# Kernel optimization log

Hardware: AMD Instinct MI355X
Metric: run time of the kernel (lower is better)

The kernel has to match this reference:

```python
import jax, jax.numpy as jnp
import numpy as np

D_MODEL = 256
D_STATE = 64
R_MIN, R_MAX, MAX_PHASE = 0.0, 1.0, 6.28


def setup_inputs() -> dict:
    key = jax.random.key(0)
    ks = jax.random.split(key, 8)
    u1 = jax.random.uniform(ks[0], (D_STATE,), dtype=jnp.float32)
    u2 = jax.random.uniform(ks[1], (D_STATE,), dtype=jnp.float32)
    nu_log = jnp.log(-0.5 * jnp.log(u1 * (R_MAX**2 - R_MIN**2) + R_MIN**2))
    theta_log = jnp.log(u2 * MAX_PHASE)
    sB = 1.0 / np.sqrt(2 * D_STATE)
    sC = 1.0 / np.sqrt(D_STATE)
    B_re = jax.random.normal(ks[2], (D_MODEL, D_STATE), dtype=jnp.float32) * sB
    B_im = jax.random.normal(ks[3], (D_MODEL, D_STATE), dtype=jnp.float32) * sB
    C_re = jax.random.normal(ks[4], (D_MODEL, D_STATE), dtype=jnp.float32) * sC
    C_im = jax.random.normal(ks[5], (D_MODEL, D_STATE), dtype=jnp.float32) * sC
    D = jax.random.normal(ks[6], (D_MODEL,), dtype=jnp.float32)
    x = jax.random.normal(ks[7], (4, 8192, D_MODEL), dtype=jnp.float32)
    return {"x": x, "nu_log": nu_log, "theta_log": theta_log,
            "B_re": B_re, "B_im": B_im, "C_re": C_re, "C_im": C_im, "D": D}


def reference(x, nu_log, theta_log, B_re, B_im, C_re, C_im, D):
    B, L, H = x.shape
    # diagonal transition: Lambda = exp(-exp(nu) + i*exp(theta)); Lambda^k = exp(k*log_lambda)
    log_lambda = -jnp.exp(nu_log) + 1j * jnp.exp(theta_log)          # (n,)
    k = jnp.arange(L, dtype=jnp.float32)
    Lambda_k = jnp.exp(k[:, None] * log_lambda[None, :])              # (L, n) complex
    CB = (C_re + 1j * C_im) * (B_re + 1j * B_im)                      # (H, n)
    kernels = jnp.einsum('hn,ln->hl', CB, Lambda_k).real              # (H, L)
    # FFT (causal, linear) convolution per channel
    n_fft = 2 * L
    x_f = jnp.fft.rfft(x, n=n_fft, axis=1)                            # (B, L+1, H)
    k_f = jnp.fft.rfft(kernels, n=n_fft, axis=1)                      # (H, L+1)
    y_f = x_f * k_f.T[None]                                           # (B, L+1, H)
    y = jnp.fft.irfft(y_f, n=n_fft, axis=1)[:, :L, :]
    return y + x * D[None, None, :]
```

## Files before the change

### kernel.cpp

```cpp
#include <hip/hip_runtime.h>
#include <hip/hip_bf16.h>

#define BB   4
#define LL   8192
#define HH   256
#define NN   64
#define NSEG 128
#define LSEG 64

typedef __attribute__((ext_vector_type(8))) short  short8;
typedef __attribute__((ext_vector_type(4))) float  float4v;
typedef __attribute__((ext_vector_type(4))) int    int4v;


__device__ __forceinline__ float ldF(const void* p, size_t i, int isbf) {
    return isbf ? __bfloat162float(((const __hip_bfloat16*)p)[i])
                : ((const float*)p)[i];
}

__global__ void k_sniff(const void* p0, const void* p1, const void* p2,
                        const void* p3, const void* p4, const void* p5,
                        const void* p6, const void* p7, int* flags)
{
    int t = threadIdx.x;
    if (t < 8) {
        const void* ps[8] = {p0, p1, p2, p3, p4, p5, p6, p7};
        const unsigned int* d = (const unsigned int*)ps[t];
        int nbf = 0, nrand = 0;
        for (int i = 0; i < 32; ++i) {
            unsigned int lo = d[i] & 0xFFFFu;
            unsigned int e  = (lo >> 7) & 0xFFu;
            if (lo == 0u) {  }
            else if (e >= 90u && e <= 140u) nbf++;
            else nrand++;
        }
        flags[t] = (nrand == 0 && nbf >= 8) ? 1 : 0;
    }
}

__global__ __launch_bounds__(256) void k_setup(
    const void* nu_log, const void* theta_log,
    const void* B_re, const void* B_im,
    const void* C_re, const void* C_im,
    const void* D, const int* __restrict__ flags,
    float* lam, float* lam64, float* Df, float* CBt,
    float* PsegRe, float* PsegIm)
{
    int t = blockIdx.x * 256 + threadIdx.x;
    if (t < NN) {
        float nu = expf(ldF(nu_log, t, flags[1]));
        float th = expf(ldF(theta_log, t, flags[2]));
        float a  = expf(-nu);
        lam[2*t]   = a * cosf(th);
        lam[2*t+1] = a * sinf(th);
        float a64 = expf(-64.0f * nu);
        float ph  = 64.0f * th;
        lam64[2*t]   = a64 * cosf(ph);
        lam64[2*t+1] = a64 * sinf(ph);
    }
    if (t < HH) Df[t] = ldF(D, t, flags[7]);
    if (t < HH * NN) {
        int h = t >> 6, n = t & 63;
        float bre = ldF(B_re, h*NN+n, flags[3]);
        float bim = ldF(B_im, h*NN+n, flags[4]);
        float cre = ldF(C_re, h*NN+n, flags[5]);
        float cim = ldF(C_im, h*NN+n, flags[6]);
        CBt[(n*2+0)*HH + h] = cre*bre - cim*bim;
        CBt[(n*2+1)*HH + h] = cre*bim + cim*bre;
    }
    if (t < 64 * 64) {
        int l = t >> 6, n = t & 63;
        float nu = expf(ldF(nu_log, n, flags[1]));
        float th = expf(ldF(theta_log, n, flags[2]));
        float fp = (float)(63 - l);
        float ar = expf(-fp * nu);
        PsegRe[t] = ar * cosf(fp * th);
        PsegIm[t] = ar * sinf(fp * th);
    }
}

__global__ __launch_bounds__(256) void k_ktab(
    const float* __restrict__ CBt, const float* __restrict__ PsegRe,
    const float* __restrict__ PsegIm, const float* __restrict__ lam64,
    float* __restrict__ Ktab,
    short* __restrict__ VreT, short* __restrict__ VimnT,
    short* __restrict__ PreH, short* __restrict__ PreL,
    short* __restrict__ PimH, short* __restrict__ PimL)
{
    int t = blockIdx.x * 256 + threadIdx.x;
    int h = t >> 6, j = t & 63;
    float acc = 0.f;
    for (int n = 0; n < NN; ++n)
        acc += CBt[(2*n)*HH + h]   * PsegRe[(63-j)*64 + n]
             - CBt[(2*n+1)*HH + h] * PsegIm[(63-j)*64 + n];
    Ktab[j*HH + h] = acc;
    if (t < 64*64) {
        int tau = t >> 6, n = t & 63;
        float vr, vi;
        if (tau < 63) {
            vr =  PsegRe[(62-tau)*64 + n];
            vi = -PsegIm[(62-tau)*64 + n];
        } else {
            vr =  lam64[2*n];
            vi = -lam64[2*n+1];
        }
        __hip_bfloat16 br = __float2bfloat16(vr);
        __hip_bfloat16 bi = __float2bfloat16(vi);
        VreT[tau*64 + n]  = *(short*)&br;
        VimnT[tau*64 + n] = *(short*)&bi;

        int n2 = t >> 6, l2 = t & 63;
        float pr = PsegRe[l2*64 + n2];
        float pi = PsegIm[l2*64 + n2];
        __hip_bfloat16 prh = __float2bfloat16(pr);
        __hip_bfloat16 prl = __float2bfloat16(pr - __bfloat162float(prh));
        __hip_bfloat16 pih = __float2bfloat16(pi);
        __hip_bfloat16 pil = __float2bfloat16(pi - __bfloat162float(pih));
        PreH[t] = *(short*)&prh;
        PreL[t] = *(short*)&prl;
        PimH[t] = *(short*)&pih;
        PimL[t] = *(short*)&pil;
    }
}

template<bool ISBF>
__device__ __forceinline__ void segsum_body(
    const void* __restrict__ x, size_t xbase,
    const short* __restrict__ PreH, const short* __restrict__ PreL,
    const short* __restrict__ PimH, const short* __restrict__ PimL,
    __hip_bfloat16* __restrict__ Abuf, size_t abase, int q, int l15)
{
    #pragma unroll
    for (int nt = 0; nt < 4; ++nt) {
        short8 xh[2], xl[2];
        #pragma unroll
        for (int ks = 0; ks < 2; ++ks)
            #pragma unroll
            for (int j = 0; j < 8; ++j) {
                size_t a = xbase + nt*16 + (size_t)(ks*32 + q*8 + j)*HH;
                if (ISBF) {
                    xh[ks][j] = ((const short*)x)[a];
                } else {
                    float xf = ((const float*)x)[a];
                    __hip_bfloat16 hv = __float2bfloat16(xf);
                    __hip_bfloat16 lv = __float2bfloat16(xf - __bfloat162float(hv));
                    xh[ks][j] = *(short*)&hv;
                    xl[ks][j] = *(short*)&lv;
                }
            }
        #pragma unroll
        for (int mt = 0; mt < 4; ++mt) {
            float4v ar = {0.f, 0.f, 0.f, 0.f};
            float4v ai = {0.f, 0.f, 0.f, 0.f};
            #pragma unroll
            for (int ks = 0; ks < 2; ++ks) {
                int off = (mt*16 + l15)*64 + ks*32 + q*8;
                short8 prh = *(const short8*)(PreH + off);
                short8 pih = *(const short8*)(PimH + off);
                short8 prl = *(const short8*)(PreL + off);
                short8 pil = *(const short8*)(PimL + off);
                ar = __builtin_amdgcn_mfma_f32_16x16x32_bf16(prh, xh[ks], ar, 0, 0, 0);
                ai = __builtin_amdgcn_mfma_f32_16x16x32_bf16(pih, xh[ks], ai, 0, 0, 0);
                ar = __builtin_amdgcn_mfma_f32_16x16x32_bf16(prl, xh[ks], ar, 0, 0, 0);
                ai = __builtin_amdgcn_mfma_f32_16x16x32_bf16(pil, xh[ks], ai, 0, 0, 0);
                if (!ISBF) {
                    ar = __builtin_amdgcn_mfma_f32_16x16x32_bf16(prh, xl[ks], ar, 0, 0, 0);
                    ai = __builtin_amdgcn_mfma_f32_16x16x32_bf16(pih, xl[ks], ai, 0, 0, 0);
                }
            }
            #pragma unroll
            for (int r = 0; r < 4; ++r) {
                int n = mt*16 + q*4 + r;
                Abuf[abase + (size_t)n*128 + nt*16 + l15]      = __float2bfloat16(ar[r]);
                Abuf[abase + (size_t)n*128 + 64 + nt*16 + l15] = __float2bfloat16(ai[r]);
            }
        }
    }
}

__global__ __launch_bounds__(256) void k_segsum(
    const void* __restrict__ x,
    const short* __restrict__ PreH, const short* __restrict__ PreL,
    const short* __restrict__ PimH, const short* __restrict__ PimL,
    const int* __restrict__ flags, __hip_bfloat16* __restrict__ Abuf)
{
    int bk = blockIdx.x;
    int s  = bk & (NSEG - 1);
    int b  = bk >> 7;
    int w    = threadIdx.x >> 6;
    int lane = threadIdx.x & 63;
    int q = lane >> 4, l15 = lane & 15;

    size_t xbase = ((size_t)(b*LL) + s*64) * HH + w*64 + l15;
    size_t abase = (((size_t)(b*4 + w) * NSEG + s) * NN) * 128;

    if (flags[0]) segsum_body<true >(x, xbase, PreH, PreL, PimH, PimL, Abuf, abase, q, l15);
    else          segsum_body<false>(x, xbase, PreH, PreL, PimH, PimL, Abuf, abase, q, l15);
}

__global__ __launch_bounds__(256) void k_scan(
    const float* __restrict__ lam64, const float* __restrict__ CBt,
    __hip_bfloat16* __restrict__ Abuf)
{
    int w    = blockIdx.x * 4 + (threadIdx.x >> 6);
    int lane = threadIdx.x & 63;
    int n    = w & 63;
    int hg   = (w >> 6) & 3;
    int b    = w >> 8;
    int h    = hg*64 + lane;

    float lre = lam64[2*n], lim = lam64[2*n+1];
    float cbre = CBt[(2*n)*HH + h], cbim = CBt[(2*n+1)*HH + h];
    float sre = 0.f, sim = 0.f;
    size_t base0 = (((size_t)(b*4 + hg) * NSEG) * NN + n) * 128 + lane;

    float curR[16], curI[16], nxtR[16], nxtI[16];
    #pragma unroll
    for (int k = 0; k < 16; ++k) {
        size_t base = base0 + (size_t)k * NN * 128;
        curR[k] = __bfloat162float(Abuf[base]);
        curI[k] = __bfloat162float(Abuf[base + 64]);
    }
    #pragma unroll
    for (int blk = 0; blk < 8; ++blk) {
        if (blk < 7) {
            #pragma unroll
            for (int k = 0; k < 16; ++k) {
                size_t base = base0 + (size_t)((blk+1)*16 + k) * NN * 128;
                nxtR[k] = __bfloat162float(Abuf[base]);
                nxtI[k] = __bfloat162float(Abuf[base + 64]);
            }
        }
        #pragma unroll
        for (int k = 0; k < 16; ++k) {
            size_t base = base0 + (size_t)(blk*16 + k) * NN * 128;
            float are = curR[k], aim = curI[k];
            float ure = cbre*sre - cbim*sim;
            float uim = cbre*sim + cbim*sre;
            Abuf[base]      = __float2bfloat16(ure);
            Abuf[base + 64] = __float2bfloat16(uim);
            float t2 = fmaf(lre, sre, fmaf(-lim, sim, are));
            sim = fmaf(lre, sim, fmaf(lim, sre, aim));
            sre = t2;
        }
        #pragma unroll
        for (int k = 0; k < 16; ++k) { curR[k] = nxtR[k]; curI[k] = nxtI[k]; }
    }
}

template<bool ISBF, int U>
__device__ __forceinline__ void conv_u(
    const void* __restrict__ x, const float* __restrict__ Df,
    const float* __restrict__ Ktab, const short* __restrict__ xs,
    const float* __restrict__ yc,
    int b, int s, int h, float* __restrict__ y)
{
    int g0 = s*64 + U*16;
    size_t rbase = ((size_t)b*LL + g0)*HH + h;
    float xv[16], yv[16];
    float dh = Df[h];
    #pragma unroll
    for (int t = 0; t < 16; ++t) {
        float xl;
        if (ISBF) xl = __bfloat162float(((const __hip_bfloat16*)x)[rbase + (size_t)t*HH]);
        else      xl = ((const float*)x)[rbase + (size_t)t*HH];
        xv[t] = xl;
        yv[t] = fmaf(dh, xl, yc[(U*16 + t)*HH + h]);
    }
    float kreg[16*U + 16];
    #pragma unroll
    for (int j = 0; j < 16*U + 16; ++j) kreg[j] = Ktab[j*HH + h];
    #pragma unroll
    for (int j = 0; j < 16; ++j)
        #pragma unroll
        for (int t = j; t < 16; ++t) yv[t] = fmaf(kreg[j], xv[t-j], yv[t]);
    #pragma unroll
    for (int m = 0; m < 16*U; ++m) {
        short bits = xs[(U*16 - 1 - m)*HH + h];
        float xm = __bfloat162float(*(const __hip_bfloat16*)&bits);
        #pragma unroll
        for (int t = 0; t < 16; ++t) yv[t] = fmaf(kreg[t+1+m], xm, yv[t]);
    }
    #pragma unroll
    for (int t = 0; t < 16; ++t) y[rbase + (size_t)t*HH] = yv[t];
}

template<bool ISBF>
__device__ __forceinline__ void cc_body(
    const short* __restrict__ VreT, const short* __restrict__ VimnT,
    const short* __restrict__ Ubuf, const void* __restrict__ x,
    const float* __restrict__ Df, const float* __restrict__ Ktab,
    float* yc, short* xs, int b, int s, float* __restrict__ y)
{
    int t = threadIdx.x;

    size_t sb = ((size_t)b*LL + s*64) * HH;
    if (ISBF) {
        const int4v* xp = (const int4v*)((const __hip_bfloat16*)x + sb);
        int4v* xd = (int4v*)xs;
        xd[t]        = xp[t];
        xd[t + 1024] = xp[t + 1024];
    } else {
        const float* xp = (const float*)x + sb;
        #pragma unroll
        for (int i = 0; i < 2; ++i) {
            int e = (t + i*1024) * 8;
            #pragma unroll
            for (int j = 0; j < 8; ++j) {
                __hip_bfloat16 v = __float2bfloat16(xp[e + j]);
                xs[e + j] = *(short*)&v;
            }
        }
    }

    int w = t >> 6, lane = t & 63;
    int hg = w & 3, nt = w >> 2;
    int q = lane >> 4, l15 = lane & 15;
    size_t ubase = (((size_t)(b*4 + hg) * NSEG + s) * NN) * 128;

    int l = nt*16 + l15;
    short8 bre[2], bim[2];
    #pragma unroll
    for (int ks = 0; ks < 2; ++ks)
        #pragma unroll
        for (int j = 0; j < 8; ++j) {
            int n = ks*32 + q*8 + j;
            bre[ks][j] = Ubuf[ubase + (size_t)n*128 + l];
            bim[ks][j] = Ubuf[ubase + (size_t)n*128 + 64 + l];
        }
    int h = hg*64 + l;
    #pragma unroll
    for (int mt = 0; mt < 4; ++mt) {
        float4v acc = {0.f, 0.f, 0.f, 0.f};
        #pragma unroll
        for (int ks = 0; ks < 2; ++ks) {
            int off = (mt*16 + l15)*64 + ks*32 + q*8;
            short8 afr = *(const short8*)(VreT + off);
            short8 afi = *(const short8*)(VimnT + off);
            acc = __builtin_amdgcn_mfma_f32_16x16x32_bf16(afr, bre[ks], acc, 0, 0, 0);
            acc = __builtin_amdgcn_mfma_f32_16x16x32_bf16(afi, bim[ks], acc, 0, 0, 0);
        }
        #pragma unroll
        for (int r = 0; r < 4; ++r) {
            int tau = mt*16 + q*4 + r;
            yc[tau*HH + h] = acc[r];
        }
    }

    __syncthreads();

    int u = w >> 2;
    int h2 = hg*64 + lane;
    switch (u) {
        case 0: conv_u<ISBF,0>(x, Df, Ktab, xs, yc, b, s, h2, y); break;
        case 1: conv_u<ISBF,1>(x, Df, Ktab, xs, yc, b, s, h2, y); break;
        case 2: conv_u<ISBF,2>(x, Df, Ktab, xs, yc, b, s, h2, y); break;
        case 3: conv_u<ISBF,3>(x, Df, Ktab, xs, yc, b, s, h2, y); break;
    }
}

__global__ __launch_bounds__(1024) void k_cc(
    const short* __restrict__ VreT, const short* __restrict__ VimnT,
    const short* __restrict__ Ubuf, const void* __restrict__ x,
    const float* __restrict__ Df, const float* __restrict__ Ktab,
    const int* __restrict__ flags, float* __restrict__ y)
{
    __shared__ float yc[64 * HH];
    __shared__ short xs[64 * HH];
    int bk = blockIdx.x;
    int s  = bk & (NSEG - 1);
    int b  = bk >> 7;
    if (flags[0]) cc_body<true >(VreT, VimnT, Ubuf, x, Df, Ktab, yc, xs, b, s, y);
    else          cc_body<false>(VreT, VimnT, Ubuf, x, Df, Ktab, yc, xs, b, s, y);
}

extern "C" void kernel_launch(void* const* d_in, const int* in_sizes, int n_in,
                              void* d_out, int out_size, void* d_ws, size_t ws_size,
                              hipStream_t stream)
{
    const void* x  = d_in[0];
    const void* nu = d_in[1];
    const void* th = d_in[2];
    const void* Br = d_in[3];
    const void* Bi = d_in[4];
    const void* Cr = d_in[5];
    const void* Ci = d_in[6];
    const void* D  = d_in[7];

    char* ws = (char*)d_ws;
    float* lam    = (float*)(ws);
    float* lam64  = (float*)(ws + 512);
    int*   flags  = (int*)(ws + 1024);
    float* Df     = (float*)(ws + 1088);
    float* CBt    = (float*)(ws + 2112);
    float* Ktab   = (float*)(ws + 133184);
    short* VreT   = (short*)(ws + 198720);
    short* VimnT  = (short*)(ws + 206912);
    float* PsegRe = (float*)(ws + 215104);
    float* PsegIm = (float*)(ws + 231744);
    short* PreH   = (short*)(ws + 248128);
    short* PreL   = (short*)(ws + 256320);
    short* PimH   = (short*)(ws + 264512);
    short* PimL   = (short*)(ws + 272704);
    __hip_bfloat16* Abuf = (__hip_bfloat16*)(ws + 294912);
    float* yout = (float*)d_out;

    k_sniff<<<dim3(1), dim3(64), 0, stream>>>(x, nu, th, Br, Bi, Cr, Ci, D, flags);
    k_setup<<<dim3(64), dim3(256), 0, stream>>>(nu, th, Br, Bi, Cr, Ci, D, flags,
                                                lam, lam64, Df, CBt, PsegRe, PsegIm);
    k_ktab<<<dim3(64), dim3(256), 0, stream>>>(CBt, PsegRe, PsegIm, lam64,
                                               Ktab, VreT, VimnT,
                                               PreH, PreL, PimH, PimL);
    k_segsum<<<dim3(512), dim3(256), 0, stream>>>(x, PreH, PreL, PimH, PimL,
                                                  flags, Abuf);
    k_scan<<<dim3(256), dim3(256), 0, stream>>>(lam64, CBt, Abuf);
    k_cc<<<dim3(512), dim3(1024), 0, stream>>>(VreT, VimnT, (const short*)Abuf,
                                               x, Df, Ktab, flags, yout);
}
```

Baseline: 188.7 us.

## Split segsum and chunk-conv kernels into finer blocks, drop shared x staging

The segment-sum kernel now runs four times as many blocks, each handling one 16-column tile instead of looping over four, which raises parallelism and occupancy. The chunk-conversion kernel is split into two 512-thread halves per segment with half the shared memory. Each half keeps the V fragments in registers and reuses them across two column tiles. The bf16 shared copy of x is removed: the intra-chunk convolution reads previous x rows straight from global memory and slides a 16-entry kernel window through registers. This cuts LDS and register pressure, at the cost of more global loads of x, which should mostly hit cache.

```diff
diff --git a/kernel.cpp b/kernel.cpp
--- a/kernel.cpp
+++ b/kernel.cpp
@@ -130,69 +130,67 @@
     const short* __restrict__ PimH, const short* __restrict__ PimL,
     __hip_bfloat16* __restrict__ Abuf, size_t abase, int q, int l15)
 {
-    #pragma unroll
-    for (int nt = 0; nt < 4; ++nt) {
-        short8 xh[2], xl[2];
-        #pragma unroll
-        for (int ks = 0; ks < 2; ++ks)
-            #pragma unroll
-            for (int j = 0; j < 8; ++j) {
-                size_t a = xbase + nt*16 + (size_t)(ks*32 + q*8 + j)*HH;
-                if (ISBF) {
-                    xh[ks][j] = ((const short*)x)[a];
-                } else {
-                    float xf = ((const float*)x)[a];
-                    __hip_bfloat16 hv = __float2bfloat16(xf);
-                    __hip_bfloat16 lv = __float2bfloat16(xf - __bfloat162float(hv));
-                    xh[ks][j] = *(short*)&hv;
-                    xl[ks][j] = *(short*)&lv;
-                }
-            }
-        #pragma unroll
-        for (int mt = 0; mt < 4; ++mt) {
-            float4v ar = {0.f, 0.f, 0.f, 0.f};
-            float4v ai = {0.f, 0.f, 0.f, 0.f};
-            #pragma unroll
-            for (int ks = 0; ks < 2; ++ks) {
-                int off = (mt*16 + l15)*64 + ks*32 + q*8;
-                short8 prh = *(const short8*)(PreH + off);
-                short8 pih = *(const short8*)(PimH + off);
-                short8 prl = *(const short8*)(PreL + off);
-                short8 pil = *(const short8*)(PimL + off);
-                ar = __builtin_amdgcn_mfma_f32_16x16x32_bf16(prh, xh[ks], ar, 0, 0, 0);
-                ai = __builtin_amdgcn_mfma_f32_16x16x32_bf16(pih, xh[ks], ai, 0, 0, 0);
-                ar = __builtin_amdgcn_mfma_f32_16x16x32_bf16(prl, xh[ks], ar, 0, 0, 0);
-                ai = __builtin_amdgcn_mfma_f32_16x16x32_bf16(pil, xh[ks], ai, 0, 0, 0);
-                if (!ISBF) {
-                    ar = __builtin_amdgcn_mfma_f32_16x16x32_bf16(prh, xl[ks], ar, 0, 0, 0);
-                    ai = __builtin_amdgcn_mfma_f32_16x16x32_bf16(pih, xl[ks], ai, 0, 0, 0);
-                }
-            }
-            #pragma unroll
-            for (int r = 0; r < 4; ++r) {
-                int n = mt*16 + q*4 + r;
-                Abuf[abase + (size_t)n*128 + nt*16 + l15]      = __float2bfloat16(ar[r]);
-                Abuf[abase + (size_t)n*128 + 64 + nt*16 + l15] = __float2bfloat16(ai[r]);
-            }
-        }
-    }
-}
-
-__global__ __launch_bounds__(256) void k_segsum(
+    short8 xh[2], xl[2];
+    #pragma unroll
+    for (int ks = 0; ks < 2; ++ks)
+        #pragma unroll
+        for (int j = 0; j < 8; ++j) {
+            size_t a = xbase + (size_t)(ks*32 + q*8 + j)*HH;
+            if (ISBF) {
+                xh[ks][j] = ((const short*)x)[a];
+            } else {
+                float xf = ((const float*)x)[a];
+                __hip_bfloat16 hv = __float2bfloat16(xf);
+                __hip_bfloat16 lv = __float2bfloat16(xf - __bfloat162float(hv));
+                xh[ks][j] = *(short*)&hv;
+                xl[ks][j] = *(short*)&lv;
+            }
+        }
+    #pragma unroll
+    for (int mt = 0; mt < 4; ++mt) {
+        float4v ar = {0.f, 0.f, 0.f, 0.f};
+        float4v ai = {0.f, 0.f, 0.f, 0.f};
+        #pragma unroll
+        for (int ks = 0; ks < 2; ++ks) {
+            int off = (mt*16 + l15)*64 + ks*32 + q*8;
+            short8 prh = *(const short8*)(PreH + off);
+            short8 pih = *(const short8*)(PimH + off);
+            short8 prl = *(const short8*)(PreL + off);
+            short8 pil = *(const short8*)(PimL + off);
+            ar = __builtin_amdgcn_mfma_f32_16x16x32_bf16(prh, xh[ks], ar, 0, 0, 0);
+            ai = __builtin_amdgcn_mfma_f32_16x16x32_bf16(pih, xh[ks], ai, 0, 0, 0);
+            ar = __builtin_amdgcn_mfma_f32_16x16x32_bf16(prl, xh[ks], ar, 0, 0, 0);
+            ai = __builtin_amdgcn_mfma_f32_16x16x32_bf16(pil, xh[ks], ai, 0, 0, 0);
+            if (!ISBF) {
+                ar = __builtin_amdgcn_mfma_f32_16x16x32_bf16(prh, xl[ks], ar, 0, 0, 0);
+                ai = __builtin_amdgcn_mfma_f32_16x16x32_bf16(pih, xl[ks], ai, 0, 0, 0);
+            }
+        }
+        #pragma unroll
+        for (int r = 0; r < 4; ++r) {
+            int n = mt*16 + q*4 + r;
+            Abuf[abase + (size_t)n*128]      = __float2bfloat16(ar[r]);
+            Abuf[abase + (size_t)n*128 + 64] = __float2bfloat16(ai[r]);
+        }
+    }
+}
+
+__global__ __launch_bounds__(256, 8) void k_segsum(
     const void* __restrict__ x,
     const short* __restrict__ PreH, const short* __restrict__ PreL,
     const short* __restrict__ PimH, const short* __restrict__ PimL,
     const int* __restrict__ flags, __hip_bfloat16* __restrict__ Abuf)
 {
     int bk = blockIdx.x;
-    int s  = bk & (NSEG - 1);
-    int b  = bk >> 7;
+    int nt = bk & 3;
+    int s  = (bk >> 2) & (NSEG - 1);
+    int b  = bk >> 9;
     int w    = threadIdx.x >> 6;
     int lane = threadIdx.x & 63;
     int q = lane >> 4, l15 = lane & 15;
 
-    size_t xbase = ((size_t)(b*LL) + s*64) * HH + w*64 + l15;
-    size_t abase = (((size_t)(b*4 + w) * NSEG + s) * NN) * 128;
+    size_t xbase = ((size_t)(b*LL) + s*64) * HH + w*64 + nt*16 + l15;
+    size_t abase = (((size_t)(b*4 + w) * NSEG + s) * NN) * 128 + nt*16 + l15;
 
     if (flags[0]) segsum_body<true >(x, xbase, PreH, PreL, PimH, PimL, Abuf, abase, q, l15);
     else          segsum_body<false>(x, xbase, PreH, PreL, PimH, PimL, Abuf, abase, q, l15);
@@ -248,14 +246,14 @@
     }
 }
 
-template<bool ISBF, int U>
+template<bool ISBF, int UU>
 __device__ __forceinline__ void conv_u(
     const void* __restrict__ x, const float* __restrict__ Df,
-    const float* __restrict__ Ktab, const short* __restrict__ xs,
-    const float* __restrict__ yc,
+    const float* __restrict__ Ktab, const float* __restrict__ yc,
     int b, int s, int h, float* __restrict__ y)
 {
-    int g0 = s*64 + U*16;
+    const int urow = UU & 1;
+    int g0 = s*64 + UU*16;
     size_t rbase = ((size_t)b*LL + g0)*HH + h;
     float xv[16], yv[16];
     float dh = Df[h];
@@ -265,21 +263,24 @@
         if (ISBF) xl = __bfloat162float(((const __hip_bfloat16*)x)[rbase + (size_t)t*HH]);
         else      xl = ((const float*)x)[rbase + (size_t)t*HH];
         xv[t] = xl;
-        yv[t] = fmaf(dh, xl, yc[(U*16 + t)*HH + h]);
-    }
-    float kreg[16*U + 16];
-    #pragma unroll
-    for (int j = 0; j < 16*U + 16; ++j) kreg[j] = Ktab[j*HH + h];
+        yv[t] = fmaf(dh, xl, yc[(urow*16 + t)*HH + h]);
+    }
+    float win[16];
+    #pragma unroll
+    for (int k = 0; k < 16; ++k) win[k] = Ktab[k*HH + h];
     #pragma unroll
     for (int j = 0; j < 16; ++j)
         #pragma unroll
-        for (int t = j; t < 16; ++t) yv[t] = fmaf(kreg[j], xv[t-j], yv[t]);
-    #pragma unroll
-    for (int m = 0; m < 16*U; ++m) {
-        short bits = xs[(U*16 - 1 - m)*HH + h];
-        float xm = __bfloat162float(*(const __hip_bfloat16*)&bits);
-        #pragma unroll
-        for (int t = 0; t < 16; ++t) yv[t] = fmaf(kreg[t+1+m], xm, yv[t]);
+        for (int t = j; t < 16; ++t) yv[t] = fmaf(win[j], xv[t-j], yv[t]);
+    #pragma unroll
+    for (int m = 0; m < 16*UU; ++m) {
+        win[m & 15] = Ktab[(m+16)*HH + h];
+        float xm;
+        size_t ra = ((size_t)b*LL + (g0 - 1 - m))*HH + h;
+        if (ISBF) xm = __bfloat162float(((const __hip_bfloat16*)x)[ra]);
+        else      xm = ((const float*)x)[ra];
+        #pragma unroll
+        for (int t = 0; t < 16; ++t) yv[t] = fmaf(win[(m+1+t) & 15], xm, yv[t]);
     }
     #pragma unroll
     for (int t = 0; t < 16; ++t) y[rbase + (size_t)t*HH] = yv[t];
@@ -290,60 +291,52 @@
     const short* __restrict__ VreT, const short* __restrict__ VimnT,
     const short* __restrict__ Ubuf, const void* __restrict__ x,
     const float* __restrict__ Df, const float* __restrict__ Ktab,
-    float* yc, short* xs, int b, int s, float* __restrict__ y)
+    float* yc, int b, int s, int half, float* __restrict__ y)
 {
     int t = threadIdx.x;
-
-    size_t sb = ((size_t)b*LL + s*64) * HH;
-    if (ISBF) {
-        const int4v* xp = (const int4v*)((const __hip_bfloat16*)x + sb);
-        int4v* xd = (int4v*)xs;
-        xd[t]        = xp[t];
-        xd[t + 1024] = xp[t + 1024];
-    } else {
-        const float* xp = (const float*)x + sb;
-        #pragma unroll
-        for (int i = 0; i < 2; ++i) {
-            int e = (t + i*1024) * 8;
+    int w = t >> 6, lane = t & 63;
+    int hg = w & 3, ntp = w >> 2;
+    int q = lane >> 4, l15 = lane & 15;
+    size_t ubase = (((size_t)(b*4 + hg) * NSEG + s) * NN) * 128;
+
+    short8 afr[2][2], afi[2][2];
+    #pragma unroll
+    for (int mtl = 0; mtl < 2; ++mtl)
+        #pragma unroll
+        for (int ks = 0; ks < 2; ++ks) {
+            int mt = half*2 + mtl;
+            int off = (mt*16 + l15)*64 + ks*32 + q*8;
+            afr[mtl][ks] = *(const short8*)(VreT + off);
+            afi[mtl][ks] = *(const short8*)(VimnT + off);
+        }
+
+    #pragma unroll
+    for (int nt2 = 0; nt2 < 2; ++nt2) {
+        int nt = ntp*2 + nt2;
+        int l = nt*16 + l15;
+        short8 bre[2], bim[2];
+        #pragma unroll
+        for (int ks = 0; ks < 2; ++ks)
             #pragma unroll
             for (int j = 0; j < 8; ++j) {
-                __hip_bfloat16 v = __float2bfloat16(xp[e + j]);
-                xs[e + j] = *(short*)&v;
-            }
-        }
-    }
-
-    int w = t >> 6, lane = t & 63;
-    int hg = w & 3, nt = w >> 2;
-    int q = lane >> 4, l15 = lane & 15;
-    size_t ubase = (((size_t)(b*4 + hg) * NSEG + s) * NN) * 128;
-
-    int l = nt*16 + l15;
-    short8 bre[2], bim[2];
-    #pragma unroll
-    for (int ks = 0; ks < 2; ++ks)
-        #pragma unroll
-        for (int j = 0; j < 8; ++j) {
-            int n = ks*32 + q*8 + j;
-            bre[ks][j] = Ubuf[ubase + (size_t)n*128 + l];
-            bim[ks][j] = Ubuf[ubase + (size_t)n*128 + 64 + l];
-        }
-    int h = hg*64 + l;
-    #pragma unroll
-    for (int mt = 0; mt < 4; ++mt) {
-        float4v acc = {0.f, 0.f, 0.f, 0.f};
-        #pragma unroll
-        for (int ks = 0; ks < 2; ++ks) {
-            int off = (mt*16 + l15)*64 + ks*32 + q*8;
-            short8 afr = *(const short8*)(VreT + off);
-            short8 afi = *(const short8*)(VimnT + off);
-            acc = __builtin_amdgcn_mfma_f32_16x16x32_bf16(afr, bre[ks], acc, 0, 0, 0);
-            acc = __builtin_amdgcn_mfma_f32_16x16x32_bf16(afi, bim[ks], acc, 0, 0, 0);
-        }
-        #pragma unroll
-        for (int r = 0; r < 4; ++r) {
-            int tau = mt*16 + q*4 + r;
-            yc[tau*HH + h] = acc[r];
+                int n = ks*32 + q*8 + j;
+                bre[ks][j] = Ubuf[ubase + (size_t)n*128 + l];
+                bim[ks][j] = Ubuf[ubase + (size_t)n*128 + 64 + l];
+            }
+        int h = hg*64 + l;
+        #pragma unroll
+        for (int mtl = 0; mtl < 2; ++mtl) {
+            float4v acc = {0.f, 0.f, 0.f, 0.f};
+            #pragma unroll
+            for (int ks = 0; ks < 2; ++ks) {
+                acc = __builtin_amdgcn_mfma_f32_16x16x32_bf16(afr[mtl][ks], bre[ks], acc, 0, 0, 0);
+                acc = __builtin_amdgcn_mfma_f32_16x16x32_bf16(afi[mtl][ks], bim[ks], acc, 0, 0, 0);
+            }
+            #pragma unroll
+            for (int r = 0; r < 4; ++r) {
+                int lrow = mtl*16 + q*4 + r;
+                yc[lrow*HH + h] = acc[r];
+            }
         }
     }
 
@@ -351,27 +344,28 @@
 
     int u = w >> 2;
     int h2 = hg*64 + lane;
-    switch (u) {
-        case 0: conv_u<ISBF,0>(x, Df, Ktab, xs, yc, b, s, h2, y); break;
-        case 1: conv_u<ISBF,1>(x, Df, Ktab, xs, yc, b, s, h2, y); break;
-        case 2: conv_u<ISBF,2>(x, Df, Ktab, xs, yc, b, s, h2, y); break;
-        case 3: conv_u<ISBF,3>(x, Df, Ktab, xs, yc, b, s, h2, y); break;
-    }
-}
-
-__global__ __launch_bounds__(1024) void k_cc(
+    int UU = half*2 + u;
+    switch (UU) {
+        case 0: conv_u<ISBF,0>(x, Df, Ktab, yc, b, s, h2, y); break;
+        case 1: conv_u<ISBF,1>(x, Df, Ktab, yc, b, s, h2, y); break;
+        case 2: conv_u<ISBF,2>(x, Df, Ktab, yc, b, s, h2, y); break;
+        case 3: conv_u<ISBF,3>(x, Df, Ktab, yc, b, s, h2, y); break;
+    }
+}
+
+__global__ __launch_bounds__(512, 4) void k_cc(
     const short* __restrict__ VreT, const short* __restrict__ VimnT,
     const short* __restrict__ Ubuf, const void* __restrict__ x,
     const float* __restrict__ Df, const float* __restrict__ Ktab,
     const int* __restrict__ flags, float* __restrict__ y)
 {
-    __shared__ float yc[64 * HH];
-    __shared__ short xs[64 * HH];
+    __shared__ float yc[32 * HH];
     int bk = blockIdx.x;
-    int s  = bk & (NSEG - 1);
-    int b  = bk >> 7;
-    if (flags[0]) cc_body<true >(VreT, VimnT, Ubuf, x, Df, Ktab, yc, xs, b, s, y);
-    else          cc_body<false>(VreT, VimnT, Ubuf, x, Df, Ktab, yc, xs, b, s, y);
+    int half = bk & 1;
+    int s  = (bk >> 1) & (NSEG - 1);
+    int b  = bk >> 8;
+    if (flags[0]) cc_body<true >(VreT, VimnT, Ubuf, x, Df, Ktab, yc, b, s, half, y);
+    else          cc_body<false>(VreT, VimnT, Ubuf, x, Df, Ktab, yc, b, s, half, y);
 }
 
 extern "C" void kernel_launch(void* const* d_in, const int* in_sizes, int n_in,
@@ -411,9 +405,9 @@
     k_ktab<<<dim3(64), dim3(256), 0, stream>>>(CBt, PsegRe, PsegIm, lam64,
                                                Ktab, VreT, VimnT,
                                                PreH, PreL, PimH, PimL);
-    k_segsum<<<dim3(512), dim3(256), 0, stream>>>(x, PreH, PreL, PimH, PimL,
-                                                  flags, Abuf);
+    k_segsum<<<dim3(2048), dim3(256), 0, stream>>>(x, PreH, PreL, PimH, PimL,
+                                                   flags, Abuf);
     k_scan<<<dim3(256), dim3(256), 0, stream>>>(lam64, CBt, Abuf);
-    k_cc<<<dim3(512), dim3(1024), 0, stream>>>(VreT, VimnT, (const short*)Abuf,
+    k_cc<<<dim3(1024), dim3(512), 0, stream>>>(VreT, VimnT, (const short*)Abuf,
                                                x, Df, Ktab, flags, yout);
 }
```

New measurement: 200.4 us. +6.2%, slower.
